# Optimization experiments

Measured on AMD Instinct MI355X. Metric: run time of the kernel, lower is better.

Reference implementation:

```python
import jax, jax.numpy as jnp
import numpy as np

N, E = 50000, 800000
D_IN, D_H, D_OUT = 128, 128, 64


def setup_inputs() -> dict:
    key = jax.random.key(0)
    ks = jax.random.split(key, 12)
    x = jax.random.normal(ks[0], (N, D_IN), dtype=jnp.float32)
    edge_index = jax.random.randint(ks[1], (2, E), 0, N, dtype=jnp.int64)
    s = 0.05
    return {
        "x": x,
        "edge_index": edge_index,
        # SAGEConv layer 0: in -> hidden. lin_l (neighbor path, with bias), lin_r (root, no bias)
        "Wl0": jax.random.normal(ks[2], (D_H, D_IN), dtype=jnp.float32) * s,
        "bl0": jnp.zeros((D_H,), dtype=jnp.float32),
        "Wr0": jax.random.normal(ks[3], (D_H, D_IN), dtype=jnp.float32) * s,
        # layer 1: hidden -> hidden
        "Wl1": jax.random.normal(ks[4], (D_H, D_H), dtype=jnp.float32) * s,
        "bl1": jnp.zeros((D_H,), dtype=jnp.float32),
        "Wr1": jax.random.normal(ks[5], (D_H, D_H), dtype=jnp.float32) * s,
        # layer 2: hidden -> out
        "Wl2": jax.random.normal(ks[6], (D_OUT, D_H), dtype=jnp.float32) * s,
        "bl2": jnp.zeros((D_OUT,), dtype=jnp.float32),
        "Wr2": jax.random.normal(ks[7], (D_OUT, D_H), dtype=jnp.float32) * s,
    }


def reference(x, edge_index, Wl0, bl0, Wr0, Wl1, bl1, Wr1, Wl2, bl2, Wr2):
    n = x.shape[0]
    src, dst = edge_index[0], edge_index[1]
    # in-degree of each target node (mean aggregation denominator)
    deg = jax.ops.segment_sum(jnp.ones_like(dst, dtype=x.dtype), dst, num_segments=n)
    inv_deg = (1.0 / jnp.maximum(deg, 1.0))[:, None]  # [N,1]; zero-degree -> sum is 0 anyway

    def sage_conv(h, Wl, bl, Wr):
        # mean-aggregate neighbor features: gather h[src], scatter-add to dst
        agg = jax.ops.segment_sum(h[src], dst, num_segments=n) * inv_deg  # [N, d]
        return agg @ Wl.T + bl + h @ Wr.T

    h = jax.nn.relu(sage_conv(x, Wl0, bl0, Wr0))
    # dropout p=0 in eval mode (training=False, force_dropout=False) -> no-op
    h = jax.nn.relu(sage_conv(h, Wl1, bl1, Wr1))
    return sage_conv(h, Wl2, bl2, Wr2)
```

## Files before the change

### kernel.cpp

```cpp
#include <hip/hip_runtime.h>


#define D_H 128
#define NBUCKET 196
#define EPB 8192
#define NBLK 98

typedef _Float16 half8  __attribute__((ext_vector_type(8)));
typedef _Float16 half4v __attribute__((ext_vector_type(4)));
typedef _Float16 half2v __attribute__((ext_vector_type(2)));
typedef float    floatx4 __attribute__((ext_vector_type(4)));

__global__ __launch_bounds__(256) void hist_kernel(const int* __restrict__ dst,
                                                   int* __restrict__ histo, int E) {
    __shared__ int h[NBUCKET];
    for (int i = threadIdx.x; i < NBUCKET; i += 256) h[i] = 0;
    __syncthreads();
    int base = blockIdx.x * EPB;
    int end = min(base + EPB, E);
    for (int i = base + threadIdx.x; i < end; i += 256)
        atomicAdd(&h[dst[i] >> 8], 1);
    __syncthreads();
    for (int i = threadIdx.x; i < NBUCKET; i += 256)
        histo[blockIdx.x * NBUCKET + i] = h[i];
}

__global__ __launch_bounds__(256) void scan_hist_kernel(const int* __restrict__ histo,
                                                        int* __restrict__ offs,
                                                        int* __restrict__ boff,
                                                        int* __restrict__ row_ptr, int n) {
    __shared__ int s[256];
    int t = threadIdx.x;
    int sum = 0;
    if (t < NBUCKET) {
        for (int b = 0; b < NBLK; ++b) {
            offs[b * NBUCKET + t] = sum;
            sum += histo[b * NBUCKET + t];
        }
    }
    s[t] = (t < NBUCKET) ? sum : 0;
    int tot = s[t];
    __syncthreads();
    for (int off = 1; off < 256; off <<= 1) {
        int tmp = (t >= off) ? s[t - off] : 0;
        __syncthreads();
        s[t] += tmp;
        __syncthreads();
    }
    int base = s[t] - tot;
    if (t < NBUCKET) boff[t] = base;
    if (t == 255) { boff[NBUCKET] = s[255]; row_ptr[n] = s[255]; }
    __syncthreads();
    if (t < NBUCKET)
        for (int b = 0; b < NBLK; ++b)
            offs[b * NBUCKET + t] += base;
}

__global__ __launch_bounds__(256) void scatter_kernel(const int* __restrict__ src,
                                                      const int* __restrict__ dst,
                                                      const int* __restrict__ offs,
                                                      unsigned int* __restrict__ bedge, int E) {
    __shared__ int lcur[NBUCKET];
    for (int i = threadIdx.x; i < NBUCKET; i += 256)
        lcur[i] = offs[blockIdx.x * NBUCKET + i];
    __syncthreads();
    int base = blockIdx.x * EPB;
    int end = min(base + EPB, E);
    for (int i = base + threadIdx.x; i < end; i += 256) {
        int d = dst[i];
        int pos = atomicAdd(&lcur[d >> 8], 1);
        bedge[pos] = ((unsigned int)(d & 255) << 16) | (unsigned int)src[i];
    }
}

__global__ __launch_bounds__(256) void bucket_build_kernel(const unsigned int* __restrict__ bedge,
                                                           const int* __restrict__ boff,
                                                           int* __restrict__ row_ptr,
                                                           float* __restrict__ inv_deg,
                                                           int* __restrict__ col, int n) {
    __shared__ int sdeg[256];
    __shared__ int sscan[256];
    __shared__ int lcur[256];
    const int b = blockIdx.x;
    const int t = threadIdx.x;
    const int base = boff[b];
    const int bend = boff[b + 1];
    sdeg[t] = 0;
    __syncthreads();
    for (int i = base + t; i < bend; i += 256)
        atomicAdd(&sdeg[bedge[i] >> 16], 1);
    __syncthreads();
    int d = sdeg[t];
    sscan[t] = d;
    __syncthreads();
    for (int off = 1; off < 256; off <<= 1) {
        int tmp = (t >= off) ? sscan[t - off] : 0;
        __syncthreads();
        sscan[t] += tmp;
        __syncthreads();
    }
    int excl = sscan[t] - d;
    int node = b * 256 + t;
    if (node < n) {
        row_ptr[node] = base + excl;
        inv_deg[node] = 1.0f / (float)max(d, 1);
    }
    lcur[t] = excl;
    __syncthreads();
    for (int i = base + t; i < bend; i += 256) {
        unsigned int v = bedge[i];
        int pos = atomicAdd(&lcur[v >> 16], 1);
        col[base + pos] = (int)(v & 0xffffu);
    }
}

__global__ __launch_bounds__(256) void convert_all_kernel(
        const float* __restrict__ x, _Float16* __restrict__ xh, int n4,
        const float* __restrict__ w0, const float* __restrict__ w1,
        const float* __restrict__ w2, const float* __restrict__ w3,
        const float* __restrict__ w4, const float* __restrict__ w5,
        _Float16* __restrict__ o0, _Float16* __restrict__ o1,
        _Float16* __restrict__ o2, _Float16* __restrict__ o3,
        _Float16* __restrict__ o4, _Float16* __restrict__ o5) {
    int i = blockIdx.x * 256 + threadIdx.x;
    const float* in; _Float16* out; int j;
    if (i < n4) { in = x; out = xh; j = i; }
    else {
        int k = i - n4;
        if      (k <  4096) { in = w0; out = o0; j = k; }
        else if (k <  8192) { in = w1; out = o1; j = k - 4096; }
        else if (k < 12288) { in = w2; out = o2; j = k - 8192; }
        else if (k < 16384) { in = w3; out = o3; j = k - 12288; }
        else if (k < 18432) { in = w4; out = o4; j = k - 16384; }
        else if (k < 20480) { in = w5; out = o5; j = k - 18432; }
        else return;
    }
    float4 v = ((const float4*)in)[j];
    half4v o = { (_Float16)v.x, (_Float16)v.y, (_Float16)v.z, (_Float16)v.w };
    ((half4v*)out)[j] = o;
}

__global__ __launch_bounds__(128, 8) void aggregate_kernel(const _Float16* __restrict__ h,
                                                           const int* __restrict__ row_ptr,
                                                           const int* __restrict__ col,
                                                           const float* __restrict__ inv_deg,
                                                           _Float16* __restrict__ agg, int n) {
    int wave = threadIdx.x >> 6;
    int lane = threadIdx.x & 63;
    int node = blockIdx.x * 2 + wave;
    if (node >= n) return;
    int beg = row_ptr[node];
    int end = row_ptr[node + 1];
    const int quarter = lane >> 4;
    const int off = (lane & 15) << 3;
    float a0f = 0.f, a1f = 0.f, a2f = 0.f, a3f = 0.f;
    float a4f = 0.f, a5f = 0.f, a6f = 0.f, a7f = 0.f;
    for (int base = beg; base < end; base += 64) {
        int m = end - base;
        if (m > 64) m = 64;
        int myc = (lane < m) ? col[base + lane] : 0;
        int t = 0;
        for (; t + 4 <= (m >> 2); t += 4) {
            int u0 = __shfl(myc, ((t + 0) << 2) + quarter);
            int u1 = __shfl(myc, ((t + 1) << 2) + quarter);
            int u2 = __shfl(myc, ((t + 2) << 2) + quarter);
            int u3 = __shfl(myc, ((t + 3) << 2) + quarter);
            half8 v0 = *(const half8*)&h[(size_t)u0 * D_H + off];
            half8 v1 = *(const half8*)&h[(size_t)u1 * D_H + off];
            half8 v2 = *(const half8*)&h[(size_t)u2 * D_H + off];
            half8 v3 = *(const half8*)&h[(size_t)u3 * D_H + off];
            a0f += (float)v0[0] + (float)v1[0] + (float)v2[0] + (float)v3[0];
            a1f += (float)v0[1] + (float)v1[1] + (float)v2[1] + (float)v3[1];
            a2f += (float)v0[2] + (float)v1[2] + (float)v2[2] + (float)v3[2];
            a3f += (float)v0[3] + (float)v1[3] + (float)v2[3] + (float)v3[3];
            a4f += (float)v0[4] + (float)v1[4] + (float)v2[4] + (float)v3[4];
            a5f += (float)v0[5] + (float)v1[5] + (float)v2[5] + (float)v3[5];
            a6f += (float)v0[6] + (float)v1[6] + (float)v2[6] + (float)v3[6];
            a7f += (float)v0[7] + (float)v1[7] + (float)v2[7] + (float)v3[7];
        }
        int smax = (m + 3) >> 2;
        for (; t < smax; ++t) {
            int j = (t << 2) + quarter;
            int u = __shfl(myc, j);
            if (j < m) {
                half8 v = *(const half8*)&h[(size_t)u * D_H + off];
                a0f += (float)v[0]; a1f += (float)v[1];
                a2f += (float)v[2]; a3f += (float)v[3];
                a4f += (float)v[4]; a5f += (float)v[5];
                a6f += (float)v[6]; a7f += (float)v[7];
            }
        }
    }
    a0f += __shfl(a0f, lane + 16); a1f += __shfl(a1f, lane + 16);
    a2f += __shfl(a2f, lane + 16); a3f += __shfl(a3f, lane + 16);
    a4f += __shfl(a4f, lane + 16); a5f += __shfl(a5f, lane + 16);
    a6f += __shfl(a6f, lane + 16); a7f += __shfl(a7f, lane + 16);
    a0f += __shfl(a0f, lane + 32); a1f += __shfl(a1f, lane + 32);
    a2f += __shfl(a2f, lane + 32); a3f += __shfl(a3f, lane + 32);
    a4f += __shfl(a4f, lane + 32); a5f += __shfl(a5f, lane + 32);
    a6f += __shfl(a6f, lane + 32); a7f += __shfl(a7f, lane + 32);
    if (quarter == 0) {
        float s = inv_deg[node];
        half8 o = { (_Float16)(a0f * s), (_Float16)(a1f * s),
                    (_Float16)(a2f * s), (_Float16)(a3f * s),
                    (_Float16)(a4f * s), (_Float16)(a5f * s),
                    (_Float16)(a6f * s), (_Float16)(a7f * s) };
        *(half8*)&agg[(size_t)node * D_H + off] = o;
    }
}

__global__ __launch_bounds__(128, 8) void aggregate_add64_kernel(
        const _Float16* __restrict__ T,
        const _Float16* __restrict__ Rh,
        const int* __restrict__ row_ptr,
        const int* __restrict__ col,
        const float* __restrict__ inv_deg,
        float* __restrict__ out, int n) {
    int wave = threadIdx.x >> 6;
    int lane = threadIdx.x & 63;
    int node = blockIdx.x * 2 + wave;
    if (node >= n) return;
    int beg = row_ptr[node];
    int end = row_ptr[node + 1];
    const int quarter = lane >> 4;
    const int off = (lane & 15) << 2;
    float a0f = 0.f, a1f = 0.f, a2f = 0.f, a3f = 0.f;
    for (int base = beg; base < end; base += 64) {
        int m = end - base;
        if (m > 64) m = 64;
        int myc = (lane < m) ? col[base + lane] : 0;
        int t = 0;
        for (; t + 4 <= (m >> 2); t += 4) {
            int u0 = __shfl(myc, ((t + 0) << 2) + quarter);
            int u1 = __shfl(myc, ((t + 1) << 2) + quarter);
            int u2 = __shfl(myc, ((t + 2) << 2) + quarter);
            int u3 = __shfl(myc, ((t + 3) << 2) + quarter);
            half4v v0 = *(const half4v*)&T[(size_t)u0 * 64 + off];
            half4v v1 = *(const half4v*)&T[(size_t)u1 * 64 + off];
            half4v v2 = *(const half4v*)&T[(size_t)u2 * 64 + off];
            half4v v3 = *(const half4v*)&T[(size_t)u3 * 64 + off];
            a0f += (float)v0[0] + (float)v1[0] + (float)v2[0] + (float)v3[0];
            a1f += (float)v0[1] + (float)v1[1] + (float)v2[1] + (float)v3[1];
            a2f += (float)v0[2] + (float)v1[2] + (float)v2[2] + (float)v3[2];
            a3f += (float)v0[3] + (float)v1[3] + (float)v2[3] + (float)v3[3];
        }
        int smax = (m + 3) >> 2;
        for (; t < smax; ++t) {
            int j = (t << 2) + quarter;
            int u = __shfl(myc, j);
            if (j < m) {
                half4v v = *(const half4v*)&T[(size_t)u * 64 + off];
                a0f += (float)v[0]; a1f += (float)v[1];
                a2f += (float)v[2]; a3f += (float)v[3];
            }
        }
    }
    a0f += __shfl(a0f, lane + 16); a1f += __shfl(a1f, lane + 16);
    a2f += __shfl(a2f, lane + 16); a3f += __shfl(a3f, lane + 16);
    a0f += __shfl(a0f, lane + 32); a1f += __shfl(a1f, lane + 32);
    a2f += __shfl(a2f, lane + 32); a3f += __shfl(a3f, lane + 32);
    if (quarter == 0) {
        float s = inv_deg[node];
        half4v r = *(const half4v*)&Rh[(size_t)node * 64 + off];
        float4 o;
        o.x = (float)r[0] + a0f * s;
        o.y = (float)r[1] + a1f * s;
        o.z = (float)r[2] + a2f * s;
        o.w = (float)r[3] + a3f * s;
        *(float4*)&out[(size_t)node * 64 + off] = o;
    }
}

template<int NT, bool RELU_HALF_OUT>
__global__ __launch_bounds__(128) void gemm_mfma_kernel(
        const _Float16* __restrict__ Xa, const _Float16* __restrict__ Xh,
        const _Float16* __restrict__ Wa, const _Float16* __restrict__ Wh,
        const float* __restrict__ bias,
        _Float16* __restrict__ out_h, float* __restrict__ out_f, int N) {
    const int wave = threadIdx.x >> 6;
    const int lane = threadIdx.x & 63;
    const int r16 = lane & 15;
    const int quad = lane >> 4;
    const int base = blockIdx.x * 64 + wave * 32;
    const int koff = quad * 8;

    floatx4 acc[2][NT];
    #pragma unroll
    for (int s = 0; s < 2; ++s)
        #pragma unroll
        for (int j = 0; j < NT; ++j)
            acc[s][j] = (floatx4){0.f, 0.f, 0.f, 0.f};

    #pragma unroll
    for (int hsel = 0; hsel < 2; ++hsel) {
        const _Float16* __restrict__ X = hsel ? Xh : Xa;
        const _Float16* __restrict__ W = hsel ? Wh : Wa;
        #pragma unroll
        for (int k0 = 0; k0 < 128; k0 += 32) {
            half8 a0 = *(const half8*)&X[(size_t)(base + r16) * 128 + k0 + koff];
            half8 a1 = *(const half8*)&X[(size_t)(base + 16 + r16) * 128 + k0 + koff];
            #pragma unroll
            for (int j = 0; j < NT; ++j) {
                half8 b = *(const half8*)&W[(size_t)(j * 16 + r16) * 128 + k0 + koff];
                acc[0][j] = __builtin_amdgcn_mfma_f32_16x16x32_f16(a0, b, acc[0][j], 0, 0, 0);
                acc[1][j] = __builtin_amdgcn_mfma_f32_16x16x32_f16(a1, b, acc[1][j], 0, 0, 0);
            }
        }
    }

    #pragma unroll
    for (int s = 0; s < 2; ++s) {
        #pragma unroll
        for (int i = 0; i < 4; ++i) {
            int r = base + s * 16 + quad * 4 + i;
            if (r >= N) continue;
            #pragma unroll
            for (int j = 0; j < NT; ++j) {
                int c = j * 16 + r16;
                float v = acc[s][j][i] + bias[c];
                if (RELU_HALF_OUT) {
                    v = fmaxf(v, 0.f);
                    out_h[(size_t)r * (NT * 16) + c] = (_Float16)v;
                } else {
                    out_f[(size_t)r * (NT * 16) + c] = v;
                }
            }
        }
    }
}

__global__ __launch_bounds__(128) void gemm_dual_kernel(
        const _Float16* __restrict__ B, const _Float16* __restrict__ Wl,
        const _Float16* __restrict__ Wr, const float* __restrict__ bias,
        _Float16* __restrict__ T, _Float16* __restrict__ Rh, int N) {
    const int wave = threadIdx.x >> 6;
    const int lane = threadIdx.x & 63;
    const int r16 = lane & 15;
    const int quad = lane >> 4;
    const int base = blockIdx.x * 64 + wave * 32;
    const int koff = quad * 8;

    floatx4 accT[2][4], accR[2][4];
    #pragma unroll
    for (int s = 0; s < 2; ++s)
        #pragma unroll
        for (int j = 0; j < 4; ++j) {
            accT[s][j] = (floatx4){0.f, 0.f, 0.f, 0.f};
            accR[s][j] = (floatx4){0.f, 0.f, 0.f, 0.f};
        }

    #pragma unroll
    for (int k0 = 0; k0 < 128; k0 += 32) {
        half8 a0 = *(const half8*)&B[(size_t)(base + r16) * 128 + k0 + koff];
        half8 a1 = *(const half8*)&B[(size_t)(base + 16 + r16) * 128 + k0 + koff];
        #pragma unroll
        for (int j = 0; j < 4; ++j) {
            half8 bl = *(const half8*)&Wl[(size_t)(j * 16 + r16) * 128 + k0 + koff];
            half8 br = *(const half8*)&Wr[(size_t)(j * 16 + r16) * 128 + k0 + koff];
            accT[0][j] = __builtin_amdgcn_mfma_f32_16x16x32_f16(a0, bl, accT[0][j], 0, 0, 0);
            accT[1][j] = __builtin_amdgcn_mfma_f32_16x16x32_f16(a1, bl, accT[1][j], 0, 0, 0);
            accR[0][j] = __builtin_amdgcn_mfma_f32_16x16x32_f16(a0, br, accR[0][j], 0, 0, 0);
            accR[1][j] = __builtin_amdgcn_mfma_f32_16x16x32_f16(a1, br, accR[1][j], 0, 0, 0);
        }
    }

    #pragma unroll
    for (int s = 0; s < 2; ++s) {
        #pragma unroll
        for (int i = 0; i < 4; ++i) {
            int r = base + s * 16 + quad * 4 + i;
            if (r >= N) continue;
            #pragma unroll
            for (int j = 0; j < 4; ++j) {
                int c = j * 16 + r16;
                T[(size_t)r * 64 + c]  = (_Float16)accT[s][j][i];
                Rh[(size_t)r * 64 + c] = (_Float16)(accR[s][j][i] + bias[c]);
            }
        }
    }
}

extern "C" void kernel_launch(void* const* d_in, const int* in_sizes, int n_in,
                              void* d_out, int out_size, void* d_ws, size_t ws_size,
                              hipStream_t stream) {
    const float* x   = (const float*)d_in[0];
    const int*   edge = (const int*)d_in[1];
    const float* Wl0 = (const float*)d_in[2];
    const float* bl0 = (const float*)d_in[3];
    const float* Wr0 = (const float*)d_in[4];
    const float* Wl1 = (const float*)d_in[5];
    const float* bl1 = (const float*)d_in[6];
    const float* Wr1 = (const float*)d_in[7];
    const float* Wl2 = (const float*)d_in[8];
    const float* bl2 = (const float*)d_in[9];
    const float* Wr2 = (const float*)d_in[10];
    float* out = (float*)d_out;

    const int N = in_sizes[0] / D_H;
    const int E = in_sizes[1] / 2;
    const int* src = edge;
    const int* dst = edge + E;

    const int gx = (N + 63) / 64;
    const int Np = gx * 64;
    const size_t HBYTES = (size_t)Np * D_H * 2;

    char* w = (char*)d_ws;
    char* P0 = w;  w += HBYTES;
    char* P1 = w;  w += HBYTES;
    char* P2 = w;  w += HBYTES;
    _Float16* Wl0h = (_Float16*)w;  w += (size_t)128 * 128 * 2;
    _Float16* Wr0h = (_Float16*)w;  w += (size_t)128 * 128 * 2;
    _Float16* Wl1h = (_Float16*)w;  w += (size_t)128 * 128 * 2;
    _Float16* Wr1h = (_Float16*)w;  w += (size_t)128 * 128 * 2;
    _Float16* Wl2h = (_Float16*)w;  w += (size_t)64 * 128 * 2;
    _Float16* Wr2h = (_Float16*)w;  w += (size_t)64 * 128 * 2;
    int* row_ptr = (int*)w;      w += (size_t)(N + 16) * 4;
    float* inv_deg = (float*)w;  w += (size_t)N * 4;
    int* col     = (int*)w;      w += (size_t)E * 4;
    int* histo   = (int*)w;      w += (size_t)NBLK * NBUCKET * 4;
    int* offs    = (int*)w;      w += (size_t)NBLK * NBUCKET * 4;
    int* boff    = (int*)w;      w += (size_t)(NBUCKET + 1) * 4;

    _Float16* xh   = (_Float16*)P0;
    _Float16* Bh   = (_Float16*)P0;
    unsigned int* bedge = (unsigned int*)P1;
    _Float16* Ah   = (_Float16*)P1;
    _Float16* aggh = (_Float16*)P2;
    _Float16* T    = (_Float16*)P2;
    _Float16* Rh   = (_Float16*)(P2 + HBYTES / 2);

    hist_kernel<<<NBLK, 256, 0, stream>>>(dst, histo, E);
    scan_hist_kernel<<<1, 256, 0, stream>>>(histo, offs, boff, row_ptr, N);
    scatter_kernel<<<NBLK, 256, 0, stream>>>(src, dst, offs, bedge, E);
    bucket_build_kernel<<<NBUCKET, 256, 0, stream>>>(bedge, boff, row_ptr, inv_deg, col, N);

    const int n4 = N * D_H / 4;
    const int ctotal = n4 + 20480;
    convert_all_kernel<<<(ctotal + 255) / 256, 256, 0, stream>>>(
        x, xh, n4, Wl0, Wr0, Wl1, Wr1, Wl2, Wr2,
        Wl0h, Wr0h, Wl1h, Wr1h, Wl2h, Wr2h);

    const int agg_grid = (N + 1) / 2;

    aggregate_kernel<<<agg_grid, 128, 0, stream>>>(xh, row_ptr, col, inv_deg, aggh, N);
    gemm_mfma_kernel<8, true><<<gx, 128, 0, stream>>>(aggh, xh, Wl0h, Wr0h, bl0, Ah, nullptr, N);

    aggregate_kernel<<<agg_grid, 128, 0, stream>>>(Ah, row_ptr, col, inv_deg, aggh, N);
    gemm_mfma_kernel<8, true><<<gx, 128, 0, stream>>>(aggh, Ah, Wl1h, Wr1h, bl1, Bh, nullptr, N);

    gemm_dual_kernel<<<gx, 128, 0, stream>>>(Bh, Wl2h, Wr2h, bl2, T, Rh, N);
    aggregate_add64_kernel<<<agg_grid, 128, 0, stream>>>(T, Rh, row_ptr, col, inv_deg, out, N);
}
```

Baseline: 295.6 us.

## Fuse neighbor aggregation into MFMA GEMM via shared memory; merge histogram and convert

Layers 0 and 1 now run a single kernel per layer. Each 64-row block first mean-aggregates its nodes' neighbors into an LDS tile and then runs the MFMA dual GEMM with bias and ReLU directly from that tile, so the fp16 agg buffer is never written to or re-read from global memory. The histogram kernel and the fp32-to-fp16 convert kernel are also merged into one launch. In exchange, only 782 blocks of 128 threads each handle the aggregation, with each wave walking 32 nodes serially, down from about 25000 small blocks. This lowers parallelism and latency hiding for the irregular gathers.

```diff
diff --git a/kernel.cpp b/kernel.cpp
--- a/kernel.cpp
+++ b/kernel.cpp
@@ -8,21 +8,46 @@
 
 typedef _Float16 half8  __attribute__((ext_vector_type(8)));
 typedef _Float16 half4v __attribute__((ext_vector_type(4)));
-typedef _Float16 half2v __attribute__((ext_vector_type(2)));
 typedef float    floatx4 __attribute__((ext_vector_type(4)));
 
-__global__ __launch_bounds__(256) void hist_kernel(const int* __restrict__ dst,
-                                                   int* __restrict__ histo, int E) {
-    __shared__ int h[NBUCKET];
-    for (int i = threadIdx.x; i < NBUCKET; i += 256) h[i] = 0;
-    __syncthreads();
-    int base = blockIdx.x * EPB;
-    int end = min(base + EPB, E);
-    for (int i = base + threadIdx.x; i < end; i += 256)
-        atomicAdd(&h[dst[i] >> 8], 1);
-    __syncthreads();
-    for (int i = threadIdx.x; i < NBUCKET; i += 256)
-        histo[blockIdx.x * NBUCKET + i] = h[i];
+__global__ __launch_bounds__(256) void hist_convert_kernel(
+        const int* __restrict__ dst, int* __restrict__ histo, int E,
+        const float* __restrict__ x, _Float16* __restrict__ xh, int n4,
+        const float* __restrict__ w0, const float* __restrict__ w1,
+        const float* __restrict__ w2, const float* __restrict__ w3,
+        const float* __restrict__ w4, const float* __restrict__ w5,
+        _Float16* __restrict__ o0, _Float16* __restrict__ o1,
+        _Float16* __restrict__ o2, _Float16* __restrict__ o3,
+        _Float16* __restrict__ o4, _Float16* __restrict__ o5) {
+    if (blockIdx.x < NBLK) {
+        __shared__ int h[NBUCKET];
+        for (int i = threadIdx.x; i < NBUCKET; i += 256) h[i] = 0;
+        __syncthreads();
+        int base = blockIdx.x * EPB;
+        int end = min(base + EPB, E);
+        for (int i = base + threadIdx.x; i < end; i += 256)
+            atomicAdd(&h[dst[i] >> 8], 1);
+        __syncthreads();
+        for (int i = threadIdx.x; i < NBUCKET; i += 256)
+            histo[blockIdx.x * NBUCKET + i] = h[i];
+        return;
+    }
+    int i = (blockIdx.x - NBLK) * 256 + threadIdx.x;
+    const float* in; _Float16* out; int j;
+    if (i < n4) { in = x; out = xh; j = i; }
+    else {
+        int k = i - n4;
+        if      (k <  4096) { in = w0; out = o0; j = k; }
+        else if (k <  8192) { in = w1; out = o1; j = k - 4096; }
+        else if (k < 12288) { in = w2; out = o2; j = k - 8192; }
+        else if (k < 16384) { in = w3; out = o3; j = k - 12288; }
+        else if (k < 18432) { in = w4; out = o4; j = k - 16384; }
+        else if (k < 20480) { in = w5; out = o5; j = k - 18432; }
+        else return;
+    }
+    float4 v = ((const float4*)in)[j];
+    half4v o = { (_Float16)v.x, (_Float16)v.y, (_Float16)v.z, (_Float16)v.w };
+    ((half4v*)out)[j] = o;
 }
 
 __global__ __launch_bounds__(256) void scan_hist_kernel(const int* __restrict__ histo,
@@ -114,98 +139,129 @@
     }
 }
 
-__global__ __launch_bounds__(256) void convert_all_kernel(
-        const float* __restrict__ x, _Float16* __restrict__ xh, int n4,
-        const float* __restrict__ w0, const float* __restrict__ w1,
-        const float* __restrict__ w2, const float* __restrict__ w3,
-        const float* __restrict__ w4, const float* __restrict__ w5,
-        _Float16* __restrict__ o0, _Float16* __restrict__ o1,
-        _Float16* __restrict__ o2, _Float16* __restrict__ o3,
-        _Float16* __restrict__ o4, _Float16* __restrict__ o5) {
-    int i = blockIdx.x * 256 + threadIdx.x;
-    const float* in; _Float16* out; int j;
-    if (i < n4) { in = x; out = xh; j = i; }
-    else {
-        int k = i - n4;
-        if      (k <  4096) { in = w0; out = o0; j = k; }
-        else if (k <  8192) { in = w1; out = o1; j = k - 4096; }
-        else if (k < 12288) { in = w2; out = o2; j = k - 8192; }
-        else if (k < 16384) { in = w3; out = o3; j = k - 12288; }
-        else if (k < 18432) { in = w4; out = o4; j = k - 16384; }
-        else if (k < 20480) { in = w5; out = o5; j = k - 18432; }
-        else return;
-    }
-    float4 v = ((const float4*)in)[j];
-    half4v o = { (_Float16)v.x, (_Float16)v.y, (_Float16)v.z, (_Float16)v.w };
-    ((half4v*)out)[j] = o;
-}
-
-__global__ __launch_bounds__(128, 8) void aggregate_kernel(const _Float16* __restrict__ h,
-                                                           const int* __restrict__ row_ptr,
-                                                           const int* __restrict__ col,
-                                                           const float* __restrict__ inv_deg,
-                                                           _Float16* __restrict__ agg, int n) {
-    int wave = threadIdx.x >> 6;
-    int lane = threadIdx.x & 63;
-    int node = blockIdx.x * 2 + wave;
-    if (node >= n) return;
-    int beg = row_ptr[node];
-    int end = row_ptr[node + 1];
+__global__ __launch_bounds__(128) void fused_agg_gemm_kernel(
+        const _Float16* __restrict__ h,
+        const int* __restrict__ row_ptr, const int* __restrict__ col,
+        const float* __restrict__ inv_deg,
+        const _Float16* __restrict__ Wa, const _Float16* __restrict__ Wh,
+        const float* __restrict__ bias,
+        _Float16* __restrict__ out_h, int N) {
+    __shared__ _Float16 aggs[64][136];
+    const int wave = threadIdx.x >> 6;
+    const int lane = threadIdx.x & 63;
     const int quarter = lane >> 4;
-    const int off = (lane & 15) << 3;
-    float a0f = 0.f, a1f = 0.f, a2f = 0.f, a3f = 0.f;
-    float a4f = 0.f, a5f = 0.f, a6f = 0.f, a7f = 0.f;
-    for (int base = beg; base < end; base += 64) {
-        int m = end - base;
-        if (m > 64) m = 64;
-        int myc = (lane < m) ? col[base + lane] : 0;
-        int t = 0;
-        for (; t + 4 <= (m >> 2); t += 4) {
-            int u0 = __shfl(myc, ((t + 0) << 2) + quarter);
-            int u1 = __shfl(myc, ((t + 1) << 2) + quarter);
-            int u2 = __shfl(myc, ((t + 2) << 2) + quarter);
-            int u3 = __shfl(myc, ((t + 3) << 2) + quarter);
-            half8 v0 = *(const half8*)&h[(size_t)u0 * D_H + off];
-            half8 v1 = *(const half8*)&h[(size_t)u1 * D_H + off];
-            half8 v2 = *(const half8*)&h[(size_t)u2 * D_H + off];
-            half8 v3 = *(const half8*)&h[(size_t)u3 * D_H + off];
-            a0f += (float)v0[0] + (float)v1[0] + (float)v2[0] + (float)v3[0];
-            a1f += (float)v0[1] + (float)v1[1] + (float)v2[1] + (float)v3[1];
-            a2f += (float)v0[2] + (float)v1[2] + (float)v2[2] + (float)v3[2];
-            a3f += (float)v0[3] + (float)v1[3] + (float)v2[3] + (float)v3[3];
-            a4f += (float)v0[4] + (float)v1[4] + (float)v2[4] + (float)v3[4];
-            a5f += (float)v0[5] + (float)v1[5] + (float)v2[5] + (float)v3[5];
-            a6f += (float)v0[6] + (float)v1[6] + (float)v2[6] + (float)v3[6];
-            a7f += (float)v0[7] + (float)v1[7] + (float)v2[7] + (float)v3[7];
-        }
-        int smax = (m + 3) >> 2;
-        for (; t < smax; ++t) {
-            int j = (t << 2) + quarter;
-            int u = __shfl(myc, j);
-            if (j < m) {
-                half8 v = *(const half8*)&h[(size_t)u * D_H + off];
-                a0f += (float)v[0]; a1f += (float)v[1];
-                a2f += (float)v[2]; a3f += (float)v[3];
-                a4f += (float)v[4]; a5f += (float)v[5];
-                a6f += (float)v[6]; a7f += (float)v[7];
+    const int r16 = lane & 15;
+    const int block0 = blockIdx.x * 64;
+
+    const int goff = r16 << 3;
+    for (int idx = 0; idx < 32; ++idx) {
+        int lrow = wave * 32 + idx;
+        int node = block0 + lrow;
+        if (node >= N) {
+            if (quarter == 0)
+                *(half8*)&aggs[lrow][goff] = (half8){0,0,0,0,0,0,0,0};
+            continue;
+        }
+        int beg = row_ptr[node];
+        int end = row_ptr[node + 1];
+        float a0f = 0.f, a1f = 0.f, a2f = 0.f, a3f = 0.f;
+        float a4f = 0.f, a5f = 0.f, a6f = 0.f, a7f = 0.f;
+        for (int base = beg; base < end; base += 64) {
+            int m = end - base;
+            if (m > 64) m = 64;
+            int myc = (lane < m) ? col[base + lane] : 0;
+            int t = 0;
+            for (; t + 4 <= (m >> 2); t += 4) {
+                int u0 = __shfl(myc, ((t + 0) << 2) + quarter);
+                int u1 = __shfl(myc, ((t + 1) << 2) + quarter);
+                int u2 = __shfl(myc, ((t + 2) << 2) + quarter);
+                int u3 = __shfl(myc, ((t + 3) << 2) + quarter);
+                half8 v0 = *(const half8*)&h[(size_t)u0 * D_H + goff];
+                half8 v1 = *(const half8*)&h[(size_t)u1 * D_H + goff];
+                half8 v2 = *(const half8*)&h[(size_t)u2 * D_H + goff];
+                half8 v3 = *(const half8*)&h[(size_t)u3 * D_H + goff];
+                a0f += (float)v0[0] + (float)v1[0] + (float)v2[0] + (float)v3[0];
+                a1f += (float)v0[1] + (float)v1[1] + (float)v2[1] + (float)v3[1];
+                a2f += (float)v0[2] + (float)v1[2] + (float)v2[2] + (float)v3[2];
+                a3f += (float)v0[3] + (float)v1[3] + (float)v2[3] + (float)v3[3];
+                a4f += (float)v0[4] + (float)v1[4] + (float)v2[4] + (float)v3[4];
+                a5f += (float)v0[5] + (float)v1[5] + (float)v2[5] + (float)v3[5];
+                a6f += (float)v0[6] + (float)v1[6] + (float)v2[6] + (float)v3[6];
+                a7f += (float)v0[7] + (float)v1[7] + (float)v2[7] + (float)v3[7];
             }
-        }
-    }
-    a0f += __shfl(a0f, lane + 16); a1f += __shfl(a1f, lane + 16);
-    a2f += __shfl(a2f, lane + 16); a3f += __shfl(a3f, lane + 16);
-    a4f += __shfl(a4f, lane + 16); a5f += __shfl(a5f, lane + 16);
-    a6f += __shfl(a6f, lane + 16); a7f += __shfl(a7f, lane + 16);
-    a0f += __shfl(a0f, lane + 32); a1f += __shfl(a1f, lane + 32);
-    a2f += __shfl(a2f, lane + 32); a3f += __shfl(a3f, lane + 32);
-    a4f += __shfl(a4f, lane + 32); a5f += __shfl(a5f, lane + 32);
-    a6f += __shfl(a6f, lane + 32); a7f += __shfl(a7f, lane + 32);
-    if (quarter == 0) {
-        float s = inv_deg[node];
-        half8 o = { (_Float16)(a0f * s), (_Float16)(a1f * s),
-                    (_Float16)(a2f * s), (_Float16)(a3f * s),
-                    (_Float16)(a4f * s), (_Float16)(a5f * s),
-                    (_Float16)(a6f * s), (_Float16)(a7f * s) };
-        *(half8*)&agg[(size_t)node * D_H + off] = o;
+            int smax = (m + 3) >> 2;
+            for (; t < smax; ++t) {
+                int j = (t << 2) + quarter;
+                int u = __shfl(myc, j);
+                if (j < m) {
+                    half8 v = *(const half8*)&h[(size_t)u * D_H + goff];
+                    a0f += (float)v[0]; a1f += (float)v[1];
+                    a2f += (float)v[2]; a3f += (float)v[3];
+                    a4f += (float)v[4]; a5f += (float)v[5];
+                    a6f += (float)v[6]; a7f += (float)v[7];
+                }
+            }
+        }
+        a0f += __shfl(a0f, lane + 16); a1f += __shfl(a1f, lane + 16);
+        a2f += __shfl(a2f, lane + 16); a3f += __shfl(a3f, lane + 16);
+        a4f += __shfl(a4f, lane + 16); a5f += __shfl(a5f, lane + 16);
+        a6f += __shfl(a6f, lane + 16); a7f += __shfl(a7f, lane + 16);
+        a0f += __shfl(a0f, lane + 32); a1f += __shfl(a1f, lane + 32);
+        a2f += __shfl(a2f, lane + 32); a3f += __shfl(a3f, lane + 32);
+        a4f += __shfl(a4f, lane + 32); a5f += __shfl(a5f, lane + 32);
+        a6f += __shfl(a6f, lane + 32); a7f += __shfl(a7f, lane + 32);
+        if (quarter == 0) {
+            float s = inv_deg[node];
+            half8 o = { (_Float16)(a0f * s), (_Float16)(a1f * s),
+                        (_Float16)(a2f * s), (_Float16)(a3f * s),
+                        (_Float16)(a4f * s), (_Float16)(a5f * s),
+                        (_Float16)(a6f * s), (_Float16)(a7f * s) };
+            *(half8*)&aggs[lrow][goff] = o;
+        }
+    }
+    __syncthreads();
+
+    const int quad = lane >> 4;
+    const int base = block0 + wave * 32;
+    const int koff = quad * 8;
+
+    floatx4 acc[2][8];
+    #pragma unroll
+    for (int s = 0; s < 2; ++s)
+        #pragma unroll
+        for (int j = 0; j < 8; ++j)
+            acc[s][j] = (floatx4){0.f, 0.f, 0.f, 0.f};
+
+    #pragma unroll
+    for (int k0 = 0; k0 < 128; k0 += 32) {
+        half8 a0 = *(const half8*)&aggs[wave * 32 + r16][k0 + koff];
+        half8 a1 = *(const half8*)&aggs[wave * 32 + 16 + r16][k0 + koff];
+        half8 c0 = *(const half8*)&h[(size_t)(base + r16) * 128 + k0 + koff];
+        half8 c1 = *(const half8*)&h[(size_t)(base + 16 + r16) * 128 + k0 + koff];
+        #pragma unroll
+        for (int j = 0; j < 8; ++j) {
+            half8 ba = *(const half8*)&Wa[(size_t)(j * 16 + r16) * 128 + k0 + koff];
+            half8 bh = *(const half8*)&Wh[(size_t)(j * 16 + r16) * 128 + k0 + koff];
+            acc[0][j] = __builtin_amdgcn_mfma_f32_16x16x32_f16(a0, ba, acc[0][j], 0, 0, 0);
+            acc[1][j] = __builtin_amdgcn_mfma_f32_16x16x32_f16(a1, ba, acc[1][j], 0, 0, 0);
+            acc[0][j] = __builtin_amdgcn_mfma_f32_16x16x32_f16(c0, bh, acc[0][j], 0, 0, 0);
+            acc[1][j] = __builtin_amdgcn_mfma_f32_16x16x32_f16(c1, bh, acc[1][j], 0, 0, 0);
+        }
+    }
+
+    #pragma unroll
+    for (int s = 0; s < 2; ++s) {
+        #pragma unroll
+        for (int i = 0; i < 4; ++i) {
+            int r = base + s * 16 + quad * 4 + i;
+            if (r >= N) continue;
+            #pragma unroll
+            for (int j = 0; j < 8; ++j) {
+                int c = j * 16 + r16;
+                float v = fmaxf(acc[s][j][i] + bias[c], 0.f);
+                out_h[(size_t)r * 128 + c] = (_Float16)v;
+            }
+        }
     }
 }
 
@@ -271,64 +327,6 @@
     }
 }
 
-template<int NT, bool RELU_HALF_OUT>
-__global__ __launch_bounds__(128) void gemm_mfma_kernel(
-        const _Float16* __restrict__ Xa, const _Float16* __restrict__ Xh,
-        const _Float16* __restrict__ Wa, const _Float16* __restrict__ Wh,
-        const float* __restrict__ bias,
-        _Float16* __restrict__ out_h, float* __restrict__ out_f, int N) {
-    const int wave = threadIdx.x >> 6;
-    const int lane = threadIdx.x & 63;
-    const int r16 = lane & 15;
-    const int quad = lane >> 4;
-    const int base = blockIdx.x * 64 + wave * 32;
-    const int koff = quad * 8;
-
-    floatx4 acc[2][NT];
-    #pragma unroll
-    for (int s = 0; s < 2; ++s)
-        #pragma unroll
-        for (int j = 0; j < NT; ++j)
-            acc[s][j] = (floatx4){0.f, 0.f, 0.f, 0.f};
-
-    #pragma unroll
-    for (int hsel = 0; hsel < 2; ++hsel) {
-        const _Float16* __restrict__ X = hsel ? Xh : Xa;
-        const _Float16* __restrict__ W = hsel ? Wh : Wa;
-        #pragma unroll
-        for (int k0 = 0; k0 < 128; k0 += 32) {
-            half8 a0 = *(const half8*)&X[(size_t)(base + r16) * 128 + k0 + koff];
-            half8 a1 = *(const half8*)&X[(size_t)(base + 16 + r16) * 128 + k0 + koff];
-            #pragma unroll
-            for (int j = 0; j < NT; ++j) {
-                half8 b = *(const half8*)&W[(size_t)(j * 16 + r16) * 128 + k0 + koff];
-                acc[0][j] = __builtin_amdgcn_mfma_f32_16x16x32_f16(a0, b, acc[0][j], 0, 0, 0);
-                acc[1][j] = __builtin_amdgcn_mfma_f32_16x16x32_f16(a1, b, acc[1][j], 0, 0, 0);
-            }
-        }
-    }
-
-    #pragma unroll
-    for (int s = 0; s < 2; ++s) {
-        #pragma unroll
-        for (int i = 0; i < 4; ++i) {
-            int r = base + s * 16 + quad * 4 + i;
-            if (r >= N) continue;
-            #pragma unroll
-            for (int j = 0; j < NT; ++j) {
-                int c = j * 16 + r16;
-                float v = acc[s][j][i] + bias[c];
-                if (RELU_HALF_OUT) {
-                    v = fmaxf(v, 0.f);
-                    out_h[(size_t)r * (NT * 16) + c] = (_Float16)v;
-                } else {
-                    out_f[(size_t)r * (NT * 16) + c] = v;
-                }
-            }
-        }
-    }
-}
-
 __global__ __launch_bounds__(128) void gemm_dual_kernel(
         const _Float16* __restrict__ B, const _Float16* __restrict__ Wl,
         const _Float16* __restrict__ Wr, const float* __restrict__ bias,
@@ -426,29 +424,27 @@
     _Float16* Bh   = (_Float16*)P0;
     unsigned int* bedge = (unsigned int*)P1;
     _Float16* Ah   = (_Float16*)P1;
-    _Float16* aggh = (_Float16*)P2;
     _Float16* T    = (_Float16*)P2;
     _Float16* Rh   = (_Float16*)(P2 + HBYTES / 2);
 
-    hist_kernel<<<NBLK, 256, 0, stream>>>(dst, histo, E);
+    const int n4 = N * D_H / 4;
+    const int conv_blocks = (n4 + 20480 + 255) / 256;
+    hist_convert_kernel<<<NBLK + conv_blocks, 256, 0, stream>>>(
+        dst, histo, E, x, xh, n4,
+        Wl0, Wr0, Wl1, Wr1, Wl2, Wr2,
+        Wl0h, Wr0h, Wl1h, Wr1h, Wl2h, Wr2h);
+
     scan_hist_kernel<<<1, 256, 0, stream>>>(histo, offs, boff, row_ptr, N);
     scatter_kernel<<<NBLK, 256, 0, stream>>>(src, dst, offs, bedge, E);
     bucket_build_kernel<<<NBUCKET, 256, 0, stream>>>(bedge, boff, row_ptr, inv_deg, col, N);
 
-    const int n4 = N * D_H / 4;
-    const int ctotal = n4 + 20480;
-    convert_all_kernel<<<(ctotal + 255) / 256, 256, 0, stream>>>(
-        x, xh, n4, Wl0, Wr0, Wl1, Wr1, Wl2, Wr2,
-        Wl0h, Wr0h, Wl1h, Wr1h, Wl2h, Wr2h);
-
-    const int agg_grid = (N + 1) / 2;
-
-    aggregate_kernel<<<agg_grid, 128, 0, stream>>>(xh, row_ptr, col, inv_deg, aggh, N);
-    gemm_mfma_kernel<8, true><<<gx, 128, 0, stream>>>(aggh, xh, Wl0h, Wr0h, bl0, Ah, nullptr, N);
-
-    aggregate_kernel<<<agg_grid, 128, 0, stream>>>(Ah, row_ptr, col, inv_deg, aggh, N);
-    gemm_mfma_kernel<8, true><<<gx, 128, 0, stream>>>(aggh, Ah, Wl1h, Wr1h, bl1, Bh, nullptr, N);
+    fused_agg_gemm_kernel<<<gx, 128, 0, stream>>>(xh, row_ptr, col, inv_deg,
+                                                  Wl0h, Wr0h, bl0, Ah, N);
+
+    fused_agg_gemm_kernel<<<gx, 128, 0, stream>>>(Ah, row_ptr, col, inv_deg,
+                                                  Wl1h, Wr1h, bl1, Bh, N);
 
     gemm_dual_kernel<<<gx, 128, 0, stream>>>(Bh, Wl2h, Wr2h, bl2, T, Rh, N);
-    aggregate_add64_kernel<<<agg_grid, 128, 0, stream>>>(T, Rh, row_ptr, col, inv_deg, out, N);
-}
+    aggregate_add64_kernel<<<(N + 1) / 2, 128, 0, stream>>>(T, Rh, row_ptr, col,
+                                                            inv_deg, out, N);
+}
```

Measured after the change: 373.8 us. 1.26x slower.
